# Performance work log

Hardware: AMD Instinct MI355X
Metric: run time of the kernel (lower is better)

Reference implementation:

```python
import jax, jax.numpy as jnp
import numpy as np

HIDDEN = 256
N_PROT = 12288
N_MOL = 6144
N_BATCH = 32


def setup_inputs() -> dict:
    key = jax.random.key(0)
    ks = jax.random.split(key, 10)
    s = 1.0 / np.sqrt(HIDDEN)  # torch Linear default init scale
    inp = {
        "prot_embed": jax.random.normal(ks[0], (N_PROT, HIDDEN), jnp.float32),
        "mol_embed": jax.random.normal(ks[1], (N_MOL, HIDDEN), jnp.float32),
        "prot_batch": jnp.sort(jax.random.randint(ks[2], (N_PROT,), 0, N_BATCH)),
        "mol_batch": jnp.sort(jax.random.randint(ks[3], (N_MOL,), 0, N_BATCH)),
        "Wq": jax.random.uniform(ks[4], (HIDDEN, HIDDEN), jnp.float32, -s, s),
        "bq": jax.random.uniform(ks[5], (HIDDEN,), jnp.float32, -s, s),
        "Wk": jax.random.uniform(ks[6], (HIDDEN, HIDDEN), jnp.float32, -s, s),
        "bk": jax.random.uniform(ks[7], (HIDDEN,), jnp.float32, -s, s),
        "Wv": jax.random.uniform(ks[8], (HIDDEN, HIDDEN), jnp.float32, -s, s),
        "bv": jax.random.uniform(ks[9], (HIDDEN,), jnp.float32, -s, s),
    }
    return inp


def reference(prot_embed, mol_embed, prot_batch, mol_batch, Wq, bq, Wk, bk, Wv, bv):
    # Linear projections (torch nn.Linear: x @ W.T + b)
    Q = prot_embed @ Wq.T + bq            # [N, H]
    K = mol_embed @ Wk.T + bk             # [M, H]
    V = mol_embed @ Wv.T + bv             # [M, H]

    scale = 1.0 / jnp.sqrt(jnp.asarray(Q.shape[-1], Q.dtype))
    scores = (Q @ K.T) * scale            # [N, M]

    # block mask: same-batch pairs only
    mask = prot_batch[:, None] == mol_batch[None, :]   # [N, M] bool
    neg_inf = jnp.asarray(-jnp.inf, scores.dtype)
    scores = jnp.where(mask, scores, neg_inf)

    # stable masked softmax; rows with no valid key -> all zeros
    # (matches torch softmax(-inf row) -> nan -> nan_to_num(0.0))
    row_any = mask.any(axis=-1, keepdims=True)
    mx = jnp.max(scores, axis=-1, keepdims=True)
    mx = jnp.where(row_any, mx, 0.0)
    e = jnp.exp(scores - mx)              # exp(-inf)=0 on masked entries
    denom = jnp.sum(e, axis=-1, keepdims=True)
    attn = e / jnp.where(row_any, denom, 1.0)  # [N, M]

    out = attn @ V                        # [N, H]
    return out, attn
```

## Files before the change

### kernel.cpp

```cpp
#include <hip/hip_runtime.h>

#define NPROT 12288
#define NMOL  6144
#define HID   256
#define NB    32

#define PROT_O 0
#define MOL_O  3145728
#define WQ_O   4718592
#define WK_O   4784128
#define WV_O   4849664
#define BQ_O   4915200
#define BK_O   4915456
#define BV_O   4915712
#define Q_O    4915968
#define K_O    8061696
#define VT_O   9634560
#define END_O  11207424

typedef __attribute__((ext_vector_type(4))) float f32x4;
typedef __attribute__((ext_vector_type(8))) short bf16x8;
typedef unsigned short u16;
typedef unsigned int   u32;

__device__ __forceinline__ float b2f(u16 u){
  union { u32 i; float f; } v; v.i = ((u32)u) << 16; return v.f;
}
__device__ __forceinline__ u16 f2b(float f){
  union { float fl; u32 i; } v; v.fl = f;
  u32 i = v.i;
  return (u16)((i + 0x7FFFu + ((i >> 16) & 1u)) >> 16);
}

__global__ __launch_bounds__(256) void convert_kernel(
    const float* __restrict__ prot, const float* __restrict__ mol,
    const float* __restrict__ Wq, const float* __restrict__ Wk,
    const float* __restrict__ Wv, const float* __restrict__ bq,
    const float* __restrict__ bk, const float* __restrict__ bv,
    const int* __restrict__ pb, const int* __restrict__ mb,
    int* __restrict__ rg, u16* __restrict__ cvt)
{
  int g = blockIdx.x * 256 + threadIdx.x;
  const float* src = nullptr; u16* dst = nullptr; int off = 0;
  if      (g < 786432)  { src = prot; dst = cvt + PROT_O; off = g; }
  else if (g < 1179648) { src = mol;  dst = cvt + MOL_O;  off = g - 786432; }
  else if (g < 1196032) { src = Wq;   dst = cvt + WQ_O;   off = g - 1179648; }
  else if (g < 1212416) { src = Wk;   dst = cvt + WK_O;   off = g - 1196032; }
  else if (g < 1228800) { src = Wv;   dst = cvt + WV_O;   off = g - 1212416; }
  else if (g < 1228864) { src = bq;   dst = cvt + BQ_O;   off = g - 1228800; }
  else if (g < 1228928) { src = bk;   dst = cvt + BK_O;   off = g - 1228864; }
  else if (g < 1228992) { src = bv;   dst = cvt + BV_O;   off = g - 1228928; }
  if (src){
    f32x4 v = *(const f32x4*)(src + (size_t)off * 4);
    ushort4 o;
    o.x = f2b(v[0]); o.y = f2b(v[1]); o.z = f2b(v[2]); o.w = f2b(v[3]);
    *(ushort4*)(dst + (size_t)off * 4) = o;
  }

  if (blockIdx.x == 0 && threadIdx.x < 64){
    int t = threadIdx.x;
    const int* arr = (t < 32) ? pb : mb;
    int n          = (t < 32) ? NPROT : NMOL;
    int target     = (t & 31) + 1;
    int lo = 0, hi = n;
    while (lo < hi){
      int mid = (lo + hi) >> 1;
      if (arr[mid] < target) lo = mid + 1; else hi = mid;
    }
    int end = lo;
    int prev = __shfl(end, t - 1);
    int start = ((t & 31) == 0) ? 0 : prev;
    int b = t & 31;
    if (t < 32){ rg[b] = start; rg[32 + b] = end; }
    else       { rg[64 + b] = start; rg[96 + b] = end; }
  }
}

__global__ __launch_bounds__(256) void proj_kernel(
    const u16* __restrict__ cvt,
    u16* __restrict__ Q, u16* __restrict__ K, u16* __restrict__ Vt)
{
  __shared__ u16 tlds[4][64][18];
  int x = blockIdx.x;
  int proj, rowblk;
  if      (x < 192){ proj = 0; rowblk = x; }
  else if (x < 288){ proj = 1; rowblk = x - 192; }
  else             { proj = 2; rowblk = x - 288; }
  const u16 *X, *W, *B;
  if (proj == 0){ X = cvt + PROT_O; W = cvt + WQ_O; B = cvt + BQ_O; }
  else if (proj == 1){ X = cvt + MOL_O; W = cvt + WK_O; B = cvt + BK_O; }
  else { X = cvt + MOL_O; W = cvt + WV_O; B = cvt + BV_O; }

  int wave = threadIdx.x >> 6, lane = threadIdx.x & 63;
  int m = lane & 15, q = lane >> 4;
  int rowbase = rowblk * 64 + wave * 16;
  int colbase = blockIdx.y * 64;

  const u16* arow = X + (size_t)(rowbase + m) * HID;
  f32x4 acc[4] = {};
  for (int k0 = 0; k0 < HID; k0 += 32){
    bf16x8 a = *(const bf16x8*)(arow + k0 + q*8);
    #pragma unroll
    for (int ct = 0; ct < 4; ct++){
      bf16x8 b = *(const bf16x8*)(W + (size_t)(colbase + ct*16 + m) * HID + k0 + q*8);
      acc[ct] = __builtin_amdgcn_mfma_f32_16x16x32_bf16(a, b, acc[ct], 0, 0, 0);
    }
  }

  if (proj < 2){
    u16* O = (proj == 0) ? Q : K;
    #pragma unroll
    for (int ct = 0; ct < 4; ct++){
      int col = colbase + ct*16 + m;
      float bb = b2f(B[col]);
      #pragma unroll
      for (int r = 0; r < 4; r++){
        int row = rowbase + q*4 + r;
        O[(size_t)row * HID + col] = f2b(acc[ct][r] + bb);
      }
    }
  } else {
    #pragma unroll
    for (int ct = 0; ct < 4; ct++){
      int lc = ct*16 + m;
      float bb = b2f(B[colbase + lc]);
      #pragma unroll
      for (int r = 0; r < 4; r++)
        tlds[wave][lc][q*4 + r] = f2b(acc[ct][r] + bb);
    }
    __syncthreads();
    int col = colbase + lane;
    u32 packed[8];
    #pragma unroll
    for (int i = 0; i < 8; i++){
      u16 lo = tlds[wave][lane][2*i];
      u16 hi = tlds[wave][lane][2*i+1];
      packed[i] = (u32)lo | ((u32)hi << 16);
    }
    u16* dst = Vt + (size_t)col * NMOL + rowbase;
    uint4 v0 = {packed[0], packed[1], packed[2], packed[3]};
    uint4 v1 = {packed[4], packed[5], packed[6], packed[7]};
    *(uint4*)dst = v0;
    *(uint4*)(dst + 8) = v1;
  }
}

__global__ __launch_bounds__(256) void attn_kernel(
    const int* __restrict__ rg, const u16* __restrict__ Q, const u16* __restrict__ K,
    const u16* __restrict__ Vt, float* __restrict__ dout)
{
  __shared__ u16 plds[4][16][48];
  __shared__ float mxw[4][16];
  __shared__ float smw[4][16];
  __shared__ float red[2][4096];
  const float scale = 0.0625f;
  int b = blockIdx.y;
  int ps = rg[b], pe = rg[32+b], ms = rg[64+b], me = rg[96+b];
  int Np = pe - ps, Nm = me - ms;
  if (Np <= 0) return;

  int wave = threadIdx.x >> 6, lane = threadIdx.x & 63;
  int m = lane & 15, q = lane >> 4;
  float* outf  = dout;
  float* attnf = dout + (size_t)NPROT * HID;
  int ntiles = (Np + 15) >> 4;

  int bs = 0, ce = 0;
  if (Nm > 0){ bs = ms & ~31; ce = bs + ((me - bs + 31) & ~31); }

  for (int tile = blockIdx.x; tile < ntiles; tile += gridDim.x){
    int row0 = ps + tile * 16;

    int qr = min(row0 + m, NPROT - 1);
    const u16* qrow = Q + (size_t)qr * HID;
    bf16x8 qf[8];
    #pragma unroll
    for (int kk = 0; kk < 8; kk++)
      qf[kk] = *(const bf16x8*)(qrow + kk*32 + q*8);

    if (Nm > 0){
      float mx[4] = {-1e30f, -1e30f, -1e30f, -1e30f};
      float sm[4] = {0.f, 0.f, 0.f, 0.f};
      for (int j0 = bs + wave*16; j0 < me; j0 += 64){
        int col = j0 + m;
        bool valid = (col >= ms) && (col < me);
        const u16* krow = K + (size_t)min(col, NMOL-1) * HID;
        f32x4 s0 = {0.f,0.f,0.f,0.f}, s1 = {0.f,0.f,0.f,0.f};
        #pragma unroll
        for (int kk = 0; kk < 4; kk++){
          bf16x8 kb0 = *(const bf16x8*)(krow + kk*32 + q*8);
          bf16x8 kb1 = *(const bf16x8*)(krow + (kk+4)*32 + q*8);
          s0 = __builtin_amdgcn_mfma_f32_16x16x32_bf16(qf[kk],   kb0, s0, 0, 0, 0);
          s1 = __builtin_amdgcn_mfma_f32_16x16x32_bf16(qf[kk+4], kb1, s1, 0, 0, 0);
        }
        f32x4 s = s0 + s1;
        float sv[4], cm[4];
        #pragma unroll
        for (int r = 0; r < 4; r++){
          sv[r] = valid ? s[r] * scale : -1e30f;
          cm[r] = sv[r];
        }
        #pragma unroll
        for (int d = 1; d < 16; d <<= 1)
          #pragma unroll
          for (int r = 0; r < 4; r++)
            cm[r] = fmaxf(cm[r], __shfl_xor(cm[r], d, 16));
        float e[4];
        #pragma unroll
        for (int r = 0; r < 4; r++){
          float mn = fmaxf(mx[r], cm[r]);
          float corr = __expf(mx[r] - mn);
          e[r] = __expf(sv[r] - mn);
          mx[r] = mn;
          sm[r] = sm[r] * corr;
        }
        #pragma unroll
        for (int d = 1; d < 16; d <<= 1)
          #pragma unroll
          for (int r = 0; r < 4; r++)
            e[r] += __shfl_xor(e[r], d, 16);
        #pragma unroll
        for (int r = 0; r < 4; r++) sm[r] += e[r];
      }
      if (m == 0){
        #pragma unroll
        for (int r = 0; r < 4; r++){
          mxw[wave][q*4 + r] = mx[r];
          smw[wave][q*4 + r] = sm[r];
        }
      }
      __syncthreads();

      float gmx[4], ginv[4];
      #pragma unroll
      for (int r = 0; r < 4; r++){
        int row = q*4 + r;
        float M = mxw[0][row];
        #pragma unroll
        for (int w = 1; w < 4; w++) M = fmaxf(M, mxw[w][row]);
        float S = 0.f;
        #pragma unroll
        for (int w = 0; w < 4; w++) S += smw[w][row] * __expf(mxw[w][row] - M);
        gmx[r] = M;
        ginv[r] = (S > 0.f) ? (1.f / S) : 0.f;
      }

      f32x4 oacc[16] = {};
      for (int j0 = bs + wave*32; j0 < ce; j0 += 128){
        #pragma unroll
        for (int sub = 0; sub < 2; sub++){
          int col = j0 + sub*16 + m;
          bool valid = (col >= ms) && (col < me);
          const u16* krow = K + (size_t)col * HID;
          f32x4 s0 = {0.f,0.f,0.f,0.f}, s1 = {0.f,0.f,0.f,0.f};
          #pragma unroll
          for (int kk = 0; kk < 4; kk++){
            bf16x8 kb0 = *(const bf16x8*)(krow + kk*32 + q*8);
            bf16x8 kb1 = *(const bf16x8*)(krow + (kk+4)*32 + q*8);
            s0 = __builtin_amdgcn_mfma_f32_16x16x32_bf16(qf[kk],   kb0, s0, 0, 0, 0);
            s1 = __builtin_amdgcn_mfma_f32_16x16x32_bf16(qf[kk+4], kb1, s1, 0, 0, 0);
          }
          f32x4 s = s0 + s1;
          #pragma unroll
          for (int r = 0; r < 4; r++){
            float pv = valid ? __expf(s[r]*scale - gmx[r]) * ginv[r] : 0.f;
            u16 pb16 = f2b(pv);
            plds[wave][q*4 + r][sub*16 + m] = pb16;
            int row = row0 + q*4 + r;
            if (valid && row < pe) attnf[(size_t)row * NMOL + col] = pv;
          }
        }
        bf16x8 a = *(const bf16x8*)(&plds[wave][m][q*8]);
        int kbase = j0 + q*8;
        #pragma unroll
        for (int ct = 0; ct < 16; ct++){
          bf16x8 vb = *(const bf16x8*)(Vt + (size_t)(ct*16 + m) * NMOL + kbase);
          oacc[ct] = __builtin_amdgcn_mfma_f32_16x16x32_bf16(a, vb, oacc[ct], 0, 0, 0);
        }
      }
      __syncthreads();

      if (wave == 1 || wave == 3){
        float* dst = red[(wave - 1) >> 1];
        #pragma unroll
        for (int ct = 0; ct < 16; ct++)
          #pragma unroll
          for (int r = 0; r < 4; r++)
            dst[(ct*4 + r)*64 + lane] = oacc[ct][r];
      }
      __syncthreads();
      if (wave == 0 || wave == 2){
        const float* src = red[wave >> 1];
        #pragma unroll
        for (int ct = 0; ct < 16; ct++)
          #pragma unroll
          for (int r = 0; r < 4; r++)
            oacc[ct][r] += src[(ct*4 + r)*64 + lane];
      }
      __syncthreads();
      if (wave == 2){
        #pragma unroll
        for (int ct = 0; ct < 16; ct++)
          #pragma unroll
          for (int r = 0; r < 4; r++)
            red[0][(ct*4 + r)*64 + lane] = oacc[ct][r];
      }
      __syncthreads();
      if (wave == 0){
        #pragma unroll
        for (int ct = 0; ct < 16; ct++){
          int colh = ct*16 + m;
          #pragma unroll
          for (int r = 0; r < 4; r++){
            float o = oacc[ct][r] + red[0][(ct*4 + r)*64 + lane];
            int row = row0 + q*4 + r;
            if (row < pe) outf[(size_t)row * HID + colh] = o;
          }
        }
      }
    } else {
      if (wave == 0){
        #pragma unroll
        for (int ct = 0; ct < 16; ct++){
          int colh = ct*16 + m;
          #pragma unroll
          for (int r = 0; r < 4; r++){
            int row = row0 + q*4 + r;
            if (row < pe) outf[(size_t)row * HID + colh] = 0.f;
          }
        }
      }
    }
    __syncthreads();
  }
}

extern "C" void kernel_launch(void* const* d_in, const int* in_sizes, int n_in,
                              void* d_out, int out_size, void* d_ws, size_t ws_size,
                              hipStream_t stream)
{
  (void)in_sizes; (void)n_in; (void)out_size;
  const float* prot = (const float*)d_in[0];
  const float* mol  = (const float*)d_in[1];
  const int* pb     = (const int*)d_in[2];
  const int* mb     = (const int*)d_in[3];
  const float* Wq   = (const float*)d_in[4];
  const float* bq   = (const float*)d_in[5];
  const float* Wk   = (const float*)d_in[6];
  const float* bk   = (const float*)d_in[7];
  const float* Wv   = (const float*)d_in[8];
  const float* bv   = (const float*)d_in[9];

  const size_t need = 1024 + (size_t)END_O * 2;
  if (ws_size < need) return;

  char* ws = (char*)d_ws;
  int* rg  = (int*)ws;
  u16* cvt = (u16*)(ws + 1024);
  u16* Qp  = cvt + Q_O;
  u16* Kp  = cvt + K_O;
  u16* Vtp = cvt + VT_O;

  hipMemsetAsync((char*)d_out + (size_t)NPROT * HID * 4, 0,
                 (size_t)NPROT * NMOL * 4, stream);
  convert_kernel<<<dim3(4801), dim3(256), 0, stream>>>(
      prot, mol, Wq, Wk, Wv, bq, bk, bv, pb, mb, rg, cvt);
  proj_kernel<<<dim3(384, 4), dim3(256), 0, stream>>>(cvt, Qp, Kp, Vtp);
  attn_kernel<<<dim3(32, NB), dim3(256), 0, stream>>>(rg, Qp, Kp, Vtp, (float*)d_out);
}
```

Baseline: 433.3 us.

## Fuse attn zero-fill into prep kernels and restructure attention softmax/PV split

```diff
diff --git a/kernel.cpp b/kernel.cpp
--- a/kernel.cpp
+++ b/kernel.cpp
@@ -18,6 +18,10 @@
 #define VT_O   9634560
 #define END_O  11207424
 
+#define FILL_BLOCKS 512
+#define FILL_CHUNK  73728
+#define FILL_HALF   37748736
+
 typedef __attribute__((ext_vector_type(4))) float f32x4;
 typedef __attribute__((ext_vector_type(8))) short bf16x8;
 typedef unsigned short u16;
@@ -30,6 +34,14 @@
   union { float fl; u32 i; } v; v.fl = f;
   u32 i = v.i;
   return (u16)((i + 0x7FFFu + ((i >> 16) & 1u)) >> 16);
+}
+
+__device__ __forceinline__ void fill_zero(float* attnf, int idx){
+  float* dst = attnf + (size_t)idx * FILL_CHUNK + threadIdx.x * 4;
+  f32x4 z = {0.f, 0.f, 0.f, 0.f};
+  #pragma unroll 4
+  for (int i = 0; i < 72; i++)
+    __builtin_nontemporal_store(z, (f32x4*)(dst + i * 1024));
 }
 
 __global__ __launch_bounds__(256) void convert_kernel(
@@ -38,8 +50,12 @@
     const float* __restrict__ Wv, const float* __restrict__ bq,
     const float* __restrict__ bk, const float* __restrict__ bv,
     const int* __restrict__ pb, const int* __restrict__ mb,
-    int* __restrict__ rg, u16* __restrict__ cvt)
+    int* __restrict__ rg, u16* __restrict__ cvt, float* __restrict__ dout)
 {
+  if (blockIdx.x >= 4801){
+    fill_zero(dout + (size_t)NPROT * HID, blockIdx.x - 4801);
+    return;
+  }
   int g = blockIdx.x * 256 + threadIdx.x;
   const float* src = nullptr; u16* dst = nullptr; int off = 0;
   if      (g < 786432)  { src = prot; dst = cvt + PROT_O; off = g; }
@@ -78,14 +94,19 @@
 
 __global__ __launch_bounds__(256) void proj_kernel(
     const u16* __restrict__ cvt,
-    u16* __restrict__ Q, u16* __restrict__ K, u16* __restrict__ Vt)
+    u16* __restrict__ Q, u16* __restrict__ K, u16* __restrict__ Vt,
+    float* __restrict__ dout)
 {
   __shared__ u16 tlds[4][64][18];
-  int x = blockIdx.x;
-  int proj, rowblk;
-  if      (x < 192){ proj = 0; rowblk = x; }
-  else if (x < 288){ proj = 1; rowblk = x - 192; }
-  else             { proj = 2; rowblk = x - 288; }
+  if (blockIdx.x >= 1536){
+    fill_zero(dout + (size_t)NPROT * HID + FILL_HALF, blockIdx.x - 1536);
+    return;
+  }
+  int rowblk = blockIdx.x >> 2, colblk = blockIdx.x & 3;
+  int proj;
+  if      (rowblk < 192){ proj = 0; }
+  else if (rowblk < 288){ proj = 1; rowblk -= 192; }
+  else                  { proj = 2; rowblk -= 288; }
   const u16 *X, *W, *B;
   if (proj == 0){ X = cvt + PROT_O; W = cvt + WQ_O; B = cvt + BQ_O; }
   else if (proj == 1){ X = cvt + MOL_O; W = cvt + WK_O; B = cvt + BK_O; }
@@ -94,7 +115,7 @@
   int wave = threadIdx.x >> 6, lane = threadIdx.x & 63;
   int m = lane & 15, q = lane >> 4;
   int rowbase = rowblk * 64 + wave * 16;
-  int colbase = blockIdx.y * 64;
+  int colbase = colblk * 64;
 
   const u16* arow = X + (size_t)(rowbase + m) * HID;
   f32x4 acc[4] = {};
@@ -149,10 +170,9 @@
     const int* __restrict__ rg, const u16* __restrict__ Q, const u16* __restrict__ K,
     const u16* __restrict__ Vt, float* __restrict__ dout)
 {
-  __shared__ u16 plds[4][16][48];
+  __shared__ u16 P[16][392];
   __shared__ float mxw[4][16];
   __shared__ float smw[4][16];
-  __shared__ float red[2][4096];
   const float scale = 0.0625f;
   int b = blockIdx.y;
   int ps = rg[b], pe = rg[32+b], ms = rg[64+b], me = rg[96+b];
@@ -170,7 +190,6 @@
 
   for (int tile = blockIdx.x; tile < ntiles; tile += gridDim.x){
     int row0 = ps + tile * 16;
-
     int qr = min(row0 + m, NPROT - 1);
     const u16* qrow = Q + (size_t)qr * HID;
     bf16x8 qf[8];
@@ -179,77 +198,14 @@
       qf[kk] = *(const bf16x8*)(qrow + kk*32 + q*8);
 
     if (Nm > 0){
+      int myj0 = bs + wave * 16;
+      f32x4 sreg[6];
       float mx[4] = {-1e30f, -1e30f, -1e30f, -1e30f};
-      float sm[4] = {0.f, 0.f, 0.f, 0.f};
-      for (int j0 = bs + wave*16; j0 < me; j0 += 64){
-        int col = j0 + m;
-        bool valid = (col >= ms) && (col < me);
-        const u16* krow = K + (size_t)min(col, NMOL-1) * HID;
-        f32x4 s0 = {0.f,0.f,0.f,0.f}, s1 = {0.f,0.f,0.f,0.f};
-        #pragma unroll
-        for (int kk = 0; kk < 4; kk++){
-          bf16x8 kb0 = *(const bf16x8*)(krow + kk*32 + q*8);
-          bf16x8 kb1 = *(const bf16x8*)(krow + (kk+4)*32 + q*8);
-          s0 = __builtin_amdgcn_mfma_f32_16x16x32_bf16(qf[kk],   kb0, s0, 0, 0, 0);
-          s1 = __builtin_amdgcn_mfma_f32_16x16x32_bf16(qf[kk+4], kb1, s1, 0, 0, 0);
-        }
-        f32x4 s = s0 + s1;
-        float sv[4], cm[4];
-        #pragma unroll
-        for (int r = 0; r < 4; r++){
-          sv[r] = valid ? s[r] * scale : -1e30f;
-          cm[r] = sv[r];
-        }
-        #pragma unroll
-        for (int d = 1; d < 16; d <<= 1)
-          #pragma unroll
-          for (int r = 0; r < 4; r++)
-            cm[r] = fmaxf(cm[r], __shfl_xor(cm[r], d, 16));
-        float e[4];
-        #pragma unroll
-        for (int r = 0; r < 4; r++){
-          float mn = fmaxf(mx[r], cm[r]);
-          float corr = __expf(mx[r] - mn);
-          e[r] = __expf(sv[r] - mn);
-          mx[r] = mn;
-          sm[r] = sm[r] * corr;
-        }
-        #pragma unroll
-        for (int d = 1; d < 16; d <<= 1)
-          #pragma unroll
-          for (int r = 0; r < 4; r++)
-            e[r] += __shfl_xor(e[r], d, 16);
-        #pragma unroll
-        for (int r = 0; r < 4; r++) sm[r] += e[r];
-      }
-      if (m == 0){
-        #pragma unroll
-        for (int r = 0; r < 4; r++){
-          mxw[wave][q*4 + r] = mx[r];
-          smw[wave][q*4 + r] = sm[r];
-        }
-      }
-      __syncthreads();
-
-      float gmx[4], ginv[4];
-      #pragma unroll
-      for (int r = 0; r < 4; r++){
-        int row = q*4 + r;
-        float M = mxw[0][row];
-        #pragma unroll
-        for (int w = 1; w < 4; w++) M = fmaxf(M, mxw[w][row]);
-        float S = 0.f;
-        #pragma unroll
-        for (int w = 0; w < 4; w++) S += smw[w][row] * __expf(mxw[w][row] - M);
-        gmx[r] = M;
-        ginv[r] = (S > 0.f) ? (1.f / S) : 0.f;
-      }
-
-      f32x4 oacc[16] = {};
-      for (int j0 = bs + wave*32; j0 < ce; j0 += 128){
-        #pragma unroll
-        for (int sub = 0; sub < 2; sub++){
-          int col = j0 + sub*16 + m;
+      #pragma unroll
+      for (int c = 0; c < 6; c++){
+        int j0 = myj0 + 64*c;
+        if (j0 < ce){
+          int col = j0 + m;
           bool valid = (col >= ms) && (col < me);
           const u16* krow = K + (size_t)col * HID;
           f32x4 s0 = {0.f,0.f,0.f,0.f}, s1 = {0.f,0.f,0.f,0.f};
@@ -260,74 +216,119 @@
             s0 = __builtin_amdgcn_mfma_f32_16x16x32_bf16(qf[kk],   kb0, s0, 0, 0, 0);
             s1 = __builtin_amdgcn_mfma_f32_16x16x32_bf16(qf[kk+4], kb1, s1, 0, 0, 0);
           }
-          f32x4 s = s0 + s1;
+          f32x4 sv;
+          #pragma unroll
+          for (int r = 0; r < 4; r++)
+            sv[r] = valid ? (s0[r] + s1[r]) * scale : -1e30f;
+          sreg[c] = sv;
+          float cm[4];
+          #pragma unroll
+          for (int r = 0; r < 4; r++) cm[r] = sv[r];
+          #pragma unroll
+          for (int d = 1; d < 16; d <<= 1)
+            #pragma unroll
+            for (int r = 0; r < 4; r++)
+              cm[r] = fmaxf(cm[r], __shfl_xor(cm[r], d, 16));
+          #pragma unroll
+          for (int r = 0; r < 4; r++) mx[r] = fmaxf(mx[r], cm[r]);
+        }
+      }
+      if (m == 0){
+        #pragma unroll
+        for (int r = 0; r < 4; r++) mxw[wave][q*4 + r] = mx[r];
+      }
+      __syncthreads();
+      float gmx[4];
+      #pragma unroll
+      for (int r = 0; r < 4; r++){
+        int row = q*4 + r;
+        float M = mxw[0][row];
+        #pragma unroll
+        for (int w = 1; w < 4; w++) M = fmaxf(M, mxw[w][row]);
+        gmx[r] = M;
+      }
+
+      float sm[4] = {0.f, 0.f, 0.f, 0.f};
+      #pragma unroll
+      for (int c = 0; c < 6; c++){
+        int j0 = myj0 + 64*c;
+        if (j0 < ce){
+          f32x4 e;
+          #pragma unroll
+          for (int r = 0; r < 4; r++) e[r] = __expf(sreg[c][r] - gmx[r]);
+          sreg[c] = e;
+          float t[4];
+          #pragma unroll
+          for (int r = 0; r < 4; r++) t[r] = e[r];
+          #pragma unroll
+          for (int d = 1; d < 16; d <<= 1)
+            #pragma unroll
+            for (int r = 0; r < 4; r++)
+              t[r] += __shfl_xor(t[r], d, 16);
+          #pragma unroll
+          for (int r = 0; r < 4; r++) sm[r] += t[r];
+        }
+      }
+      if (m == 0){
+        #pragma unroll
+        for (int r = 0; r < 4; r++) smw[wave][q*4 + r] = sm[r];
+      }
+      __syncthreads();
+      float ginv[4];
+      #pragma unroll
+      for (int r = 0; r < 4; r++){
+        int row = q*4 + r;
+        float S = smw[0][row] + smw[1][row] + smw[2][row] + smw[3][row];
+        ginv[r] = (S > 0.f) ? (1.f / S) : 0.f;
+      }
+
+      #pragma unroll
+      for (int c = 0; c < 6; c++){
+        int j0 = myj0 + 64*c;
+        if (j0 < ce){
+          int col = j0 + m;
+          int jl = j0 - bs;
+          bool valid = (col >= ms) && (col < me);
           #pragma unroll
           for (int r = 0; r < 4; r++){
-            float pv = valid ? __expf(s[r]*scale - gmx[r]) * ginv[r] : 0.f;
-            u16 pb16 = f2b(pv);
-            plds[wave][q*4 + r][sub*16 + m] = pb16;
+            float p = sreg[c][r] * ginv[r];
+            P[q*4 + r][jl + m] = f2b(p);
             int row = row0 + q*4 + r;
-            if (valid && row < pe) attnf[(size_t)row * NMOL + col] = pv;
+            if (valid && row < pe)
+              __builtin_nontemporal_store(p, attnf + (size_t)row * NMOL + col);
           }
         }
-        bf16x8 a = *(const bf16x8*)(&plds[wave][m][q*8]);
-        int kbase = j0 + q*8;
-        #pragma unroll
-        for (int ct = 0; ct < 16; ct++){
-          bf16x8 vb = *(const bf16x8*)(Vt + (size_t)(ct*16 + m) * NMOL + kbase);
-          oacc[ct] = __builtin_amdgcn_mfma_f32_16x16x32_bf16(a, vb, oacc[ct], 0, 0, 0);
-        }
       }
       __syncthreads();
 
-      if (wave == 1 || wave == 3){
-        float* dst = red[(wave - 1) >> 1];
-        #pragma unroll
-        for (int ct = 0; ct < 16; ct++)
-          #pragma unroll
-          for (int r = 0; r < 4; r++)
-            dst[(ct*4 + r)*64 + lane] = oacc[ct][r];
-      }
-      __syncthreads();
-      if (wave == 0 || wave == 2){
-        const float* src = red[wave >> 1];
-        #pragma unroll
-        for (int ct = 0; ct < 16; ct++)
-          #pragma unroll
-          for (int r = 0; r < 4; r++)
-            oacc[ct][r] += src[(ct*4 + r)*64 + lane];
-      }
-      __syncthreads();
-      if (wave == 2){
-        #pragma unroll
-        for (int ct = 0; ct < 16; ct++)
-          #pragma unroll
-          for (int r = 0; r < 4; r++)
-            red[0][(ct*4 + r)*64 + lane] = oacc[ct][r];
-      }
-      __syncthreads();
-      if (wave == 0){
-        #pragma unroll
-        for (int ct = 0; ct < 16; ct++){
-          int colh = ct*16 + m;
-          #pragma unroll
-          for (int r = 0; r < 4; r++){
-            float o = oacc[ct][r] + red[0][(ct*4 + r)*64 + lane];
-            int row = row0 + q*4 + r;
-            if (row < pe) outf[(size_t)row * HID + colh] = o;
-          }
+      f32x4 oacc[4] = {};
+      for (int j0 = bs; j0 < ce; j0 += 32){
+        int jl = j0 - bs;
+        bf16x8 a = *(const bf16x8*)(&P[m][jl + q*8]);
+        #pragma unroll
+        for (int c2 = 0; c2 < 4; c2++){
+          int ct = wave*4 + c2;
+          bf16x8 vb = *(const bf16x8*)(Vt + (size_t)(ct*16 + m) * NMOL + j0 + q*8);
+          oacc[c2] = __builtin_amdgcn_mfma_f32_16x16x32_bf16(a, vb, oacc[c2], 0, 0, 0);
+        }
+      }
+      #pragma unroll
+      for (int c2 = 0; c2 < 4; c2++){
+        int col = (wave*4 + c2)*16 + m;
+        #pragma unroll
+        for (int r = 0; r < 4; r++){
+          int row = row0 + q*4 + r;
+          if (row < pe) outf[(size_t)row * HID + col] = oacc[c2][r];
         }
       }
     } else {
-      if (wave == 0){
-        #pragma unroll
-        for (int ct = 0; ct < 16; ct++){
-          int colh = ct*16 + m;
-          #pragma unroll
-          for (int r = 0; r < 4; r++){
-            int row = row0 + q*4 + r;
-            if (row < pe) outf[(size_t)row * HID + colh] = 0.f;
-          }
+      #pragma unroll
+      for (int c2 = 0; c2 < 4; c2++){
+        int col = (wave*4 + c2)*16 + m;
+        #pragma unroll
+        for (int r = 0; r < 4; r++){
+          int row = row0 + q*4 + r;
+          if (row < pe) outf[(size_t)row * HID + col] = 0.f;
         }
       }
     }
@@ -360,11 +361,11 @@
   u16* Qp  = cvt + Q_O;
   u16* Kp  = cvt + K_O;
   u16* Vtp = cvt + VT_O;
-
-  hipMemsetAsync((char*)d_out + (size_t)NPROT * HID * 4, 0,
-                 (size_t)NPROT * NMOL * 4, stream);
-  convert_kernel<<<dim3(4801), dim3(256), 0, stream>>>(
-      prot, mol, Wq, Wk, Wv, bq, bk, bv, pb, mb, rg, cvt);
-  proj_kernel<<<dim3(384, 4), dim3(256), 0, stream>>>(cvt, Qp, Kp, Vtp);
-  attn_kernel<<<dim3(32, NB), dim3(256), 0, stream>>>(rg, Qp, Kp, Vtp, (float*)d_out);
-}
+  float* out = (float*)d_out;
+
+  convert_kernel<<<dim3(4801 + FILL_BLOCKS), dim3(256), 0, stream>>>(
+      prot, mol, Wq, Wk, Wv, bq, bk, bv, pb, mb, rg, cvt, out);
+  proj_kernel<<<dim3(1536 + FILL_BLOCKS), dim3(256), 0, stream>>>(
+      cvt, Qp, Kp, Vtp, out);
+  attn_kernel<<<dim3(32, NB), dim3(256), 0, stream>>>(rg, Qp, Kp, Vtp, out);
+}
```

Result: faster. 407.4 us (-6.0%).
